# Optimization experiments

Hardware: AMD Instinct MI355X
Metric: run time of the kernel (lower is better)

## Reference

```python
import jax, jax.numpy as jnp
import numpy as np

EPS = 1e-6
T, B, E, H, D, P = 1024, 4, 512, 8, 64, 64  # tgt_len, bsz, embed_dim, heads, head_dim, proj_dim


def setup_inputs() -> dict:
    key = jax.random.key(0)
    ks = jax.random.split(key, 8)
    wscale = (2.0 / (E + E)) ** 0.5  # xavier-ish, gain=init_scale**-0.5=1
    return {
        "x": jax.random.normal(ks[0], (T, B, E), jnp.float32),
        "random_matrices": jax.random.normal(ks[1], (H, P, D), jnp.float32),
        "Wq": jax.random.normal(ks[2], (E, E), jnp.float32) * wscale,
        "bq": jnp.zeros((E,), jnp.float32),
        "Wk": jax.random.normal(ks[3], (E, E), jnp.float32) * wscale,
        "bk": jnp.zeros((E,), jnp.float32),
        "Wv": jax.random.normal(ks[4], (E, E), jnp.float32) * wscale,
        "bv": jnp.zeros((E,), jnp.float32),
        "Wo": jax.random.normal(ks[5], (E, E), jnp.float32) * wscale,
        "bo": jnp.zeros((E,), jnp.float32),
    }


def _phi(x, rm, tau=1.0):
    # RFA trig random features: l2-normalize (scaled by 1/tau), project with
    # per-head random matrices, then [sin, cos] / sqrt(proj_dim).
    # x: [T,B,H,D], rm: [H,P,D] -> [T,B,H,2P]
    xn = x / (tau * jnp.maximum(jnp.linalg.norm(x, axis=-1, keepdims=True), EPS))
    proj = jnp.einsum('tbhd,hpd->tbhp', xn, rm)
    return jnp.concatenate([jnp.sin(proj), jnp.cos(proj)], axis=-1) * (P ** -0.5)


def reference(x, random_matrices, Wq, bq, Wk, bk, Wv, bv, Wo, bo):
    t, b, e = x.shape
    q = (x @ Wq.T + bq).reshape(t, b, H, D)
    k = (x @ Wk.T + bk).reshape(t, b, H, D)
    v = (x @ Wv.T + bv).reshape(t, b, H, D)

    pq = _phi(q, random_matrices)  # [T,B,H,2P]
    pk = _phi(k, random_matrices)  # [T,B,H,2P]

    K = 2 * P
    s0 = jnp.zeros((b, H, K, D), x.dtype)
    z0 = jnp.zeros((b, H, K), x.dtype)

    def step(carry, inp):
        s, z = carry
        pq_t, pk_t, v_t = inp  # [B,H,K], [B,H,K], [B,H,D]
        s = s + pk_t[..., :, None] * v_t[..., None, :]   # outer(phi_k, v)
        z = z + pk_t
        qs = jnp.einsum('bhk,bhkd->bhd', pq_t, s)
        qz = jnp.maximum(jnp.einsum('bhk,bhk->bh', pq_t, z), EPS)
        return (s, z), qs / qz[..., None]

    _, attn = jax.lax.scan(step, (s0, z0), (pq, pk, v))  # attn: [T,B,H,D]
    attn = attn.reshape(t, b, e)
    return attn @ Wo.T + bo
```

## Files before the change

### kernel.cpp

```cpp
#include <hip/hip_runtime.h>

#define T_ 1024
#define B_ 4
#define E_ 512
#define H_ 8
#define D_ 64
#define P_ 64
#define K2 128
#define N_ (T_*B_)
#define CHK 64
#define NC (T_/CHK)
#define BH (B_*H_)
#define EPSV 1e-6f

typedef unsigned int uint;
typedef unsigned short ushort;
typedef short short8 __attribute__((ext_vector_type(8)));
typedef float f32x4 __attribute__((ext_vector_type(4)));

__device__ __forceinline__ float b2f(ushort u){ return __uint_as_float(((uint)u) << 16); }
__device__ __forceinline__ ushort f2b(float f){
  uint x = __float_as_uint(f);
  return (ushort)((x + 0x7fffu + ((x >> 16) & 1u)) >> 16);
}
__device__ __forceinline__ float lo16(uint u){ return __uint_as_float(u << 16); }
__device__ __forceinline__ float hi16(uint u){ return __uint_as_float(u & 0xffff0000u); }
__device__ __forceinline__ void st(float* p, float v){ *p = v; }
__device__ __forceinline__ void st(ushort* p, float v){ *p = f2b(v); }

__device__ __forceinline__ void gl16(const ushort* g, ushort* lds) {
  __builtin_amdgcn_global_load_lds(
      (const __attribute__((address_space(1))) uint*)g,
      (__attribute__((address_space(3))) uint*)lds, 16, 0, 0);
}

__global__ __launch_bounds__(256) void cast_kernel(
    const float* __restrict__ x, const float* __restrict__ wq, const float* __restrict__ wk,
    const float* __restrict__ wv, const float* __restrict__ wo, const float* __restrict__ rm,
    ushort* __restrict__ xb, ushort* __restrict__ wqb, ushort* __restrict__ wkb,
    ushort* __restrict__ wvb, ushort* __restrict__ wob, ushort* __restrict__ rmb)
{
  const float* src; ushort* dst; int n4;
  switch (blockIdx.y) {
    case 0:  src = x;  dst = xb;  n4 = N_ * E_ / 4; break;
    case 1:  src = wq; dst = wqb; n4 = E_ * E_ / 4; break;
    case 2:  src = wk; dst = wkb; n4 = E_ * E_ / 4; break;
    case 3:  src = wv; dst = wvb; n4 = E_ * E_ / 4; break;
    case 4:  src = wo; dst = wob; n4 = E_ * E_ / 4; break;
    default: src = rm; dst = rmb; n4 = H_ * P_ * D_ / 4; break;
  }
  const int stride = gridDim.x * 256;
  for (int i = blockIdx.x * 256 + threadIdx.x; i < n4; i += stride) {
    const float4 v = *(const float4*)(src + (size_t)i * 4);
    ushort4 o; o.x = f2b(v.x); o.y = f2b(v.y); o.z = f2b(v.z); o.w = f2b(v.w);
    *(ushort4*)(dst + (size_t)i * 4) = o;
  }
}

template<typename OutT>
__device__ __forceinline__ void gemm_tile(
    const ushort* __restrict__ A, const ushort* __restrict__ W,
    const float* __restrict__ bias, OutT* __restrict__ out,
    const int row0, const int col0)
{
  __shared__ ushort sA[128 * 32];
  __shared__ ushort sB[64 * 32];
  const int tid = threadIdx.x, w = tid >> 6, lane = tid & 63;
  const int lrow = lane >> 2, lk8 = (lane & 3) * 8;
  const ushort* gA = A + (size_t)(row0 + w * 16 + lrow) * E_ + lk8;
  const ushort* gB = W + (size_t)(col0 + w * 16 + lrow) * E_ + lk8;
  ushort* lA = sA + w * 512;
  ushort* lB = sB + w * 512;
  const int r = lane & 15, kg = lane >> 4, kq = kg * 8;
  f32x4 acc[4][4] = {};
  for (int k0 = 0; k0 < E_; k0 += 32) {
    gl16(gA + k0,             lA);
    gl16(gA + k0 + 32 * E_,   lA + 1024);
    gl16(gA + k0 + 64 * E_,   lA + 2048);
    gl16(gA + k0 + 96 * E_,   lA + 3072);
    gl16(gB + k0,             lB);
    gl16(gB + k0 + 32 * E_,   lB + 1024);
    __syncthreads();
    short8 af[4], bf[4];
    #pragma unroll
    for (int m = 0; m < 4; ++m) af[m] = *(const short8*)(sA + (w * 64 + m * 16 + r) * 32 + kq);
    #pragma unroll
    for (int n = 0; n < 4; ++n) bf[n] = *(const short8*)(sB + (n * 16 + r) * 32 + kq);
    #pragma unroll
    for (int m = 0; m < 4; ++m)
      #pragma unroll
      for (int n = 0; n < 4; ++n)
        acc[m][n] = __builtin_amdgcn_mfma_f32_16x16x32_bf16(af[m], bf[n], acc[m][n], 0, 0, 0);
    __syncthreads();
  }
  float bs[4];
  #pragma unroll
  for (int n = 0; n < 4; ++n) bs[n] = bias[col0 + n * 16 + r];
  #pragma unroll
  for (int m = 0; m < 4; ++m) {
    #pragma unroll
    for (int j = 0; j < 4; ++j) {
      const int row_g = row0 + w * 64 + m * 16 + kg * 4 + j;
      #pragma unroll
      for (int n = 0; n < 4; ++n)
        st(out + (size_t)row_g * E_ + col0 + n * 16 + r, acc[m][n][j] + bs[n]);
    }
  }
}

__global__ __launch_bounds__(128) void gemm_qkv_kernel(
    const ushort* __restrict__ A,
    const ushort* __restrict__ wq, const ushort* __restrict__ wk, const ushort* __restrict__ wv,
    const float* __restrict__ bq, const float* __restrict__ bk, const float* __restrict__ bv,
    ushort* __restrict__ qb, ushort* __restrict__ kb, ushort* __restrict__ vb)
{
  const ushort* W; const float* bias; ushort* dst;
  if (blockIdx.z == 0)      { W = wq; bias = bq; dst = qb; }
  else if (blockIdx.z == 1) { W = wk; bias = bk; dst = kb; }
  else                      { W = wv; bias = bv; dst = vb; }
  gemm_tile<ushort>(A, W, bias, dst, blockIdx.x * 128, blockIdx.y * 64);
}

__global__ __launch_bounds__(128) void gemm_out_kernel(
    const ushort* __restrict__ A, const ushort* __restrict__ W,
    const float* __restrict__ bias, float* __restrict__ out)
{
  gemm_tile<float>(A, W, bias, out, blockIdx.x * 128, blockIdx.y * 64);
}

__global__ __launch_bounds__(256) void phi_kernel(
    const ushort* __restrict__ qb, const ushort* __restrict__ kb,
    const ushort* __restrict__ rmb, ushort* __restrict__ pq, ushort* __restrict__ pk)
{
  __shared__ ushort xq[64][72];
  __shared__ ushort rms[64][72];
  __shared__ float inv_s[64];
  const int tid = threadIdx.x;
  const int h = blockIdx.y;
  const ushort* src = blockIdx.z ? kb : qb;
  ushort* dst = blockIdx.z ? pk : pq;
  const int n0 = blockIdx.x * 64;
  const int row = tid >> 2, seg = (tid & 3) * 16;
  {
    const ushort* gq = src + (size_t)(n0 + row) * E_ + h * D_ + seg;
    const ushort* gr = rmb + ((size_t)h * P_ + row) * D_ + seg;
    const uint4 q0 = *(const uint4*)(gq);
    const uint4 q1 = *(const uint4*)(gq + 8);
    *(uint4*)(&xq[row][seg])      = q0;
    *(uint4*)(&xq[row][seg + 8])  = q1;
    *(uint4*)(&rms[row][seg])     = *(const uint4*)(gr);
    *(uint4*)(&rms[row][seg + 8]) = *(const uint4*)(gr + 8);
    float s2 = 0.f;
    const uint* qw = (const uint*)&q0;
    #pragma unroll
    for (int i = 0; i < 4; ++i) { const float a = lo16(qw[i]), b = hi16(qw[i]); s2 += a*a + b*b; }
    const uint* qw1 = (const uint*)&q1;
    #pragma unroll
    for (int i = 0; i < 4; ++i) { const float a = lo16(qw1[i]), b = hi16(qw1[i]); s2 += a*a + b*b; }
    s2 += __shfl_xor(s2, 1, 64);
    s2 += __shfl_xor(s2, 2, 64);
    if ((tid & 3) == 0) inv_s[row] = 1.0f / fmaxf(sqrtf(s2), EPSV);
  }
  __syncthreads();
  const int w = tid >> 6, lane = tid & 63;
  const int r = lane & 15, kg = lane >> 4;
  const int m0 = w * 16;
  f32x4 acc[4] = {};
  #pragma unroll
  for (int k0 = 0; k0 < D_; k0 += 32) {
    const short8 a = *(const short8*)(&xq[m0 + r][k0 + kg * 8]);
    #pragma unroll
    for (int nt = 0; nt < 4; ++nt) {
      const short8 bfr = *(const short8*)(&rms[nt * 16 + r][k0 + kg * 8]);
      acc[nt] = __builtin_amdgcn_mfma_f32_16x16x32_bf16(a, bfr, acc[nt], 0, 0, 0);
    }
  }
  #pragma unroll
  for (int j = 0; j < 4; ++j) {
    const int rr = m0 + kg * 4 + j;
    const float inv = inv_s[rr];
    const size_t base = ((size_t)(n0 + rr) * H_ + h) * K2;
    #pragma unroll
    for (int nt = 0; nt < 4; ++nt) {
      const int p = nt * 16 + r;
      const float proj = acc[nt][j] * inv;
      dst[base + p]      = f2b(__sinf(proj) * 0.125f);
      dst[base + 64 + p] = f2b(__cosf(proj) * 0.125f);
    }
  }
}

__global__ __launch_bounds__(256) void chunk_sum_kernel(
    const ushort* __restrict__ pk, const ushort* __restrict__ v,
    ushort* __restrict__ cS, float* __restrict__ cz)
{
  const int c = blockIdx.x, bh = blockIdx.y, b = bh >> 3, h = bh & 7;
  __shared__ ushort pkT[K2][88];
  __shared__ ushort vT[D_][88];
  const int tid = threadIdx.x;
  for (int i = tid; i < CHK * 16; i += 256) {
    const int tt = i >> 4, k8 = (i & 15) * 8;
    const int n = (c * CHK + tt) * B_ + b;
    const ushort4 u0 = *(const ushort4*)(pk + ((size_t)n * H_ + h) * K2 + k8);
    const ushort4 u1 = *(const ushort4*)(pk + ((size_t)n * H_ + h) * K2 + k8 + 4);
    pkT[k8+0][tt] = u0.x; pkT[k8+1][tt] = u0.y; pkT[k8+2][tt] = u0.z; pkT[k8+3][tt] = u0.w;
    pkT[k8+4][tt] = u1.x; pkT[k8+5][tt] = u1.y; pkT[k8+6][tt] = u1.z; pkT[k8+7][tt] = u1.w;
  }
  for (int i = tid; i < CHK * 16; i += 256) {
    const int tt = i >> 4, d4 = (i & 15) * 4;
    const int n = (c * CHK + tt) * B_ + b;
    const ushort4 u = *(const ushort4*)(v + (size_t)n * E_ + h * D_ + d4);
    vT[d4+0][tt] = u.x; vT[d4+1][tt] = u.y; vT[d4+2][tt] = u.z; vT[d4+3][tt] = u.w;
  }
  __syncthreads();
  const int w = tid >> 6, lane = tid & 63;
  const int r = lane & 15, kb = lane >> 4;
  const int m0 = w * 32;
  f32x4 acc[2][4] = {};
  #pragma unroll
  for (int k0 = 0; k0 < CHK; k0 += 32) {
    const short8 a0 = *(const short8*)(&pkT[m0 + r][k0 + kb * 8]);
    const short8 a1 = *(const short8*)(&pkT[m0 + 16 + r][k0 + kb * 8]);
    #pragma unroll
    for (int nt = 0; nt < 4; ++nt) {
      const short8 bv = *(const short8*)(&vT[nt * 16 + r][k0 + kb * 8]);
      acc[0][nt] = __builtin_amdgcn_mfma_f32_16x16x32_bf16(a0, bv, acc[0][nt], 0, 0, 0);
      acc[1][nt] = __builtin_amdgcn_mfma_f32_16x16x32_bf16(a1, bv, acc[1][nt], 0, 0, 0);
    }
  }
  ushort* So = cS + (size_t)(c * BH + bh) * (K2 * D_);
  #pragma unroll
  for (int mt = 0; mt < 2; ++mt)
    #pragma unroll
    for (int nt = 0; nt < 4; ++nt)
      #pragma unroll
      for (int j = 0; j < 4; ++j)
        So[(m0 + mt * 16 + kb * 4 + j) * D_ + nt * 16 + r] = f2b(acc[mt][nt][j]);
  if (tid < K2) {
    float zacc = 0.f;
    #pragma unroll
    for (int i2 = 0; i2 < CHK / 2; ++i2) {
      const uint u = *(const uint*)(&pkT[tid][i2 * 2]);
      zacc += lo16(u) + hi16(u);
    }
    cz[(size_t)(c * BH + bh) * K2 + tid] = zacc;
  }
}

__global__ __launch_bounds__(256) void prefix_kernel(
    ushort* __restrict__ cS, float* __restrict__ cz)
{
  const int gid = blockIdx.x * 256 + threadIdx.x;
  const int bh = gid >> 13, rem = gid & 8191;
  float run = 0.f;
  #pragma unroll
  for (int c = 0; c < NC; ++c) {
    ushort* p = cS + (((size_t)(c * BH + bh)) << 13) + rem;
    const float t = b2f(*p); *p = f2b(run); run += t;
  }
  if (gid < BH * K2) {
    const int zbh = gid >> 7, k2 = gid & 127;
    float rz = 0.f;
    #pragma unroll
    for (int c = 0; c < NC; ++c) {
      float* pz = cz + (size_t)(c * BH + zbh) * K2 + k2;
      const float t = *pz; *pz = rz; rz += t;
    }
  }
}

__global__ __launch_bounds__(256) void chunk_out_kernel(
    const ushort* __restrict__ pq, const ushort* __restrict__ pkg,
    const ushort* __restrict__ v, const ushort* __restrict__ Sp,
    const float* __restrict__ zp, ushort* __restrict__ attn)
{
  const int c = blockIdx.x, bh = blockIdx.y, b = bh >> 3, h = bh & 7;
  __shared__ ushort pq_s[CHK][136];
  __shared__ ushort pk_s[CHK][136];
  __shared__ ushort SpT_s[D_][136];
  __shared__ ushort vT_s[D_][88];
  __shared__ ushort Am_s[CHK][88];
  __shared__ float zps[K2];
  __shared__ float dens_s[CHK];
  __shared__ float inv_s[CHK];
  const int tid = threadIdx.x;
  for (int i = tid; i < CHK * 16; i += 256) {
    const int tt = i >> 4, k8 = (i & 15) * 8;
    const int n = (c * CHK + tt) * B_ + b;
    const size_t off = ((size_t)n * H_ + h) * K2 + k8;
    *(uint4*)(&pq_s[tt][k8]) = *(const uint4*)(pq + off);
    *(uint4*)(&pk_s[tt][k8]) = *(const uint4*)(pkg + off);
  }
  for (int i = tid; i < CHK * 16; i += 256) {
    const int tt = i >> 4, d4 = (i & 15) * 4;
    const int n = (c * CHK + tt) * B_ + b;
    const ushort4 u = *(const ushort4*)(v + (size_t)n * E_ + h * D_ + d4);
    vT_s[d4+0][tt] = u.x; vT_s[d4+1][tt] = u.y; vT_s[d4+2][tt] = u.z; vT_s[d4+3][tt] = u.w;
  }
  const ushort* Spb = Sp + (size_t)(c * BH + bh) * (K2 * D_);
  for (int i = tid; i < K2 * 8; i += 256) {
    const int k2 = i >> 3, d8 = (i & 7) * 8;
    const ushort4 s0 = *(const ushort4*)(Spb + k2 * D_ + d8);
    const ushort4 s1 = *(const ushort4*)(Spb + k2 * D_ + d8 + 4);
    SpT_s[d8+0][k2] = s0.x; SpT_s[d8+1][k2] = s0.y;
    SpT_s[d8+2][k2] = s0.z; SpT_s[d8+3][k2] = s0.w;
    SpT_s[d8+4][k2] = s1.x; SpT_s[d8+5][k2] = s1.y;
    SpT_s[d8+6][k2] = s1.z; SpT_s[d8+7][k2] = s1.w;
  }
  if (tid < K2) zps[tid] = zp[(size_t)(c * BH + bh) * K2 + tid];
  __syncthreads();

  const int w = tid >> 6, lane = tid & 63;
  const int r = lane & 15, kb = lane >> 4;
  const int m0 = w * 16;
  f32x4 accA[4] = {};
  #pragma unroll
  for (int k0 = 0; k0 < K2; k0 += 32) {
    const short8 aq = *(const short8*)(&pq_s[m0 + r][k0 + kb * 8]);
    #pragma unroll
    for (int nt = 0; nt < 4; ++nt) {
      const short8 bk = *(const short8*)(&pk_s[nt * 16 + r][k0 + kb * 8]);
      accA[nt] = __builtin_amdgcn_mfma_f32_16x16x32_bf16(aq, bk, accA[nt], 0, 0, 0);
    }
  }
  float rs[4] = {0.f, 0.f, 0.f, 0.f};
  #pragma unroll
  for (int nt = 0; nt < 4; ++nt) {
    #pragma unroll
    for (int j = 0; j < 4; ++j) {
      const int row = kb * 4 + j, col = nt * 16 + r;
      float a = accA[nt][j];
      a = (col <= m0 + row) ? a : 0.f;
      rs[j] += a;
      Am_s[m0 + row][col] = f2b(a);
    }
  }
  #pragma unroll
  for (int off = 1; off < 16; off <<= 1) {
    rs[0] += __shfl_xor(rs[0], off, 64);
    rs[1] += __shfl_xor(rs[1], off, 64);
    rs[2] += __shfl_xor(rs[2], off, 64);
    rs[3] += __shfl_xor(rs[3], off, 64);
  }
  if (r == 0) {
    #pragma unroll
    for (int j = 0; j < 4; ++j) dens_s[m0 + kb * 4 + j] = rs[j];
  }
  f32x4 accO[4] = {};
  #pragma unroll
  for (int k0 = 0; k0 < CHK; k0 += 32) {
    const short8 aa = *(const short8*)(&Am_s[m0 + r][k0 + kb * 8]);
    #pragma unroll
    for (int nt = 0; nt < 4; ++nt) {
      const short8 bv = *(const short8*)(&vT_s[nt * 16 + r][k0 + kb * 8]);
      accO[nt] = __builtin_amdgcn_mfma_f32_16x16x32_bf16(aa, bv, accO[nt], 0, 0, 0);
    }
  }
  #pragma unroll
  for (int k0 = 0; k0 < K2; k0 += 32) {
    const short8 aq = *(const short8*)(&pq_s[m0 + r][k0 + kb * 8]);
    #pragma unroll
    for (int nt = 0; nt < 4; ++nt) {
      const short8 bs = *(const short8*)(&SpT_s[nt * 16 + r][k0 + kb * 8]);
      accO[nt] = __builtin_amdgcn_mfma_f32_16x16x32_bf16(aq, bs, accO[nt], 0, 0, 0);
    }
  }
  {
    const int t_loc = m0 + (lane >> 2), seg = lane & 3;
    float qz = 0.f;
    #pragma unroll
    for (int ii = 0; ii < 16; ++ii) {
      const uint u = *(const uint*)(&pq_s[t_loc][seg * 32 + ii * 2]);
      qz += lo16(u) * zps[seg * 32 + ii * 2] + hi16(u) * zps[seg * 32 + ii * 2 + 1];
    }
    qz += __shfl_xor(qz, 1, 64);
    qz += __shfl_xor(qz, 2, 64);
    if (seg == 0) inv_s[t_loc] = 1.0f / fmaxf(dens_s[t_loc] + qz, EPSV);
  }
  #pragma unroll
  for (int j = 0; j < 4; ++j) {
    const int row = m0 + kb * 4 + j;
    const float inv = inv_s[row];
    const int n = (c * CHK + row) * B_ + b;
    ushort* op = attn + (size_t)n * E_ + h * D_;
    #pragma unroll
    for (int nt = 0; nt < 4; ++nt) op[nt * 16 + r] = f2b(accO[nt][j] * inv);
  }
}

extern "C" void kernel_launch(void* const* d_in, const int* in_sizes, int n_in,
                              void* d_out, int out_size, void* d_ws, size_t ws_size,
                              hipStream_t stream) {
  const float* x  = (const float*)d_in[0];
  const float* rm = (const float*)d_in[1];
  const float* Wq = (const float*)d_in[2];
  const float* bq = (const float*)d_in[3];
  const float* Wk = (const float*)d_in[4];
  const float* bk = (const float*)d_in[5];
  const float* Wv = (const float*)d_in[6];
  const float* bv = (const float*)d_in[7];
  const float* Wo = (const float*)d_in[8];
  const float* bo = (const float*)d_in[9];
  float* out = (float*)d_out;

  ushort* xb  = (ushort*)d_ws;
  ushort* wqb = xb + (size_t)N_ * E_;
  ushort* wkb = wqb + (size_t)E_ * E_;
  ushort* wvb = wkb + (size_t)E_ * E_;
  ushort* wob = wvb + (size_t)E_ * E_;
  ushort* rmb = wob + (size_t)E_ * E_;
  ushort* qb  = rmb + (size_t)H_ * P_ * D_;
  ushort* kb  = qb + (size_t)N_ * E_;
  ushort* vb  = kb + (size_t)N_ * E_;
  ushort* pqb = vb + (size_t)N_ * E_;
  ushort* pkb = pqb + (size_t)N_ * H_ * K2;
  ushort* attnb = pkb + (size_t)N_ * H_ * K2;
  ushort* cS = attnb + (size_t)N_ * E_;
  float* cz = (float*)(cS + (size_t)NC * BH * K2 * D_);

  cast_kernel<<<dim3(512, 6), dim3(256), 0, stream>>>(
      x, Wq, Wk, Wv, Wo, rm, xb, wqb, wkb, wvb, wob, rmb);
  gemm_qkv_kernel<<<dim3(N_ / 128, E_ / 64, 3), dim3(128), 0, stream>>>(
      xb, wqb, wkb, wvb, bq, bk, bv, qb, kb, vb);
  phi_kernel<<<dim3(N_ / 64, H_, 2), dim3(256), 0, stream>>>(qb, kb, rmb, pqb, pkb);
  chunk_sum_kernel<<<dim3(NC, BH), dim3(256), 0, stream>>>(pkb, vb, cS, cz);
  prefix_kernel<<<dim3(1024), dim3(256), 0, stream>>>(cS, cz);
  chunk_out_kernel<<<dim3(NC, BH), dim3(256), 0, stream>>>(pqb, pkb, vb, cS, cz, attnb);
  gemm_out_kernel<<<dim3(N_ / 128, E_ / 64), dim3(128), 0, stream>>>(attnb, wob, bo, out);
}
```

Before: 63.47 us.

## Fuse phi feature map into QKV projection GEMM epilogue

The Q/K projection GEMM now computes the per-head L2 norm and the random-feature projection with sin/cos inside its epilogue. Because each block's 64-column tile is exactly one head, the Q and K intermediates no longer need to be written to global memory and read back. This removes one kernel launch and the global round trip of q and k. In exchange the GEMM kernel uses more shared memory and registers, and the norm is now taken over fp32 values rather than rounded bf16 values.

```diff
diff --git a/kernel.cpp b/kernel.cpp
--- a/kernel.cpp
+++ b/kernel.cpp
@@ -57,14 +57,25 @@
   }
 }
 
-template<typename OutT>
-__device__ __forceinline__ void gemm_tile(
-    const ushort* __restrict__ A, const ushort* __restrict__ W,
-    const float* __restrict__ bias, OutT* __restrict__ out,
-    const int row0, const int col0)
-{
-  __shared__ ushort sA[128 * 32];
-  __shared__ ushort sB[64 * 32];
+__global__ __launch_bounds__(128) void gemm_qkv_phi_kernel(
+    const ushort* __restrict__ A,
+    const ushort* __restrict__ wq, const ushort* __restrict__ wk, const ushort* __restrict__ wv,
+    const float* __restrict__ bq, const float* __restrict__ bk, const float* __restrict__ bv,
+    const ushort* __restrict__ rmb,
+    ushort* __restrict__ vb, ushort* __restrict__ pq, ushort* __restrict__ pk)
+{
+  __shared__ ushort smem[14080];
+  ushort* sA = smem;
+  ushort* sB = smem + 4096;
+  const int z = blockIdx.z;
+  const ushort* W; const float* bias;
+  if (z == 0)      { W = wq; bias = bq; }
+  else if (z == 1) { W = wk; bias = bk; }
+  else             { W = wv; bias = bv; }
+  const int row0 = blockIdx.x * 128;
+  const int h = blockIdx.y;
+  const int col0 = h * 64;
+
   const int tid = threadIdx.x, w = tid >> 6, lane = tid & 63;
   const int lrow = lane >> 2, lk8 = (lane & 3) * 8;
   const ushort* gA = A + (size_t)(row0 + w * 16 + lrow) * E_ + lk8;
@@ -96,98 +107,137 @@
   float bs[4];
   #pragma unroll
   for (int n = 0; n < 4; ++n) bs[n] = bias[col0 + n * 16 + r];
-  #pragma unroll
-  for (int m = 0; m < 4; ++m) {
+
+  if (z == 2) {
+    #pragma unroll
+    for (int m = 0; m < 4; ++m)
+      #pragma unroll
+      for (int j = 0; j < 4; ++j) {
+        const int row_g = row0 + w * 64 + m * 16 + kg * 4 + j;
+        #pragma unroll
+        for (int n = 0; n < 4; ++n)
+          vb[(size_t)row_g * E_ + col0 + n * 16 + r] = f2b(acc[m][n][j] + bs[n]);
+      }
+    return;
+  }
+
+  ushort* qt    = smem;
+  ushort* rms   = smem + 9216;
+  float*  inv_s = (float*)(smem + 13824);
+  {
+    const int rrow = tid >> 1, half = (tid & 1) * 32;
+    const ushort* gr = rmb + ((size_t)h * P_ + rrow) * D_ + half;
+    ushort* dr = rms + rrow * 72 + half;
+    *(uint4*)(dr)      = *(const uint4*)(gr);
+    *(uint4*)(dr + 8)  = *(const uint4*)(gr + 8);
+    *(uint4*)(dr + 16) = *(const uint4*)(gr + 16);
+    *(uint4*)(dr + 24) = *(const uint4*)(gr + 24);
+  }
+  float rs[16];
+  #pragma unroll
+  for (int i = 0; i < 16; ++i) rs[i] = 0.f;
+  #pragma unroll
+  for (int m = 0; m < 4; ++m)
+    #pragma unroll
+    for (int nt = 0; nt < 4; ++nt)
+      #pragma unroll
+      for (int j = 0; j < 4; ++j) {
+        const float val = acc[m][nt][j] + bs[nt];
+        qt[(w * 64 + m * 16 + kg * 4 + j) * 72 + nt * 16 + r] = f2b(val);
+        rs[m * 4 + j] += val * val;
+      }
+  #pragma unroll
+  for (int off = 1; off < 16; off <<= 1)
+    #pragma unroll
+    for (int i = 0; i < 16; ++i) rs[i] += __shfl_xor(rs[i], off, 64);
+  if (r == 0) {
+    #pragma unroll
+    for (int m = 0; m < 4; ++m)
+      #pragma unroll
+      for (int j = 0; j < 4; ++j)
+        inv_s[w * 64 + m * 16 + kg * 4 + j] = 1.0f / fmaxf(sqrtf(rs[m * 4 + j]), EPSV);
+  }
+  __syncthreads();
+  f32x4 acc2[4][4] = {};
+  #pragma unroll
+  for (int k0 = 0; k0 < D_; k0 += 32) {
+    short8 af2[4];
+    #pragma unroll
+    for (int m = 0; m < 4; ++m)
+      af2[m] = *(const short8*)(&qt[(w * 64 + m * 16 + r) * 72 + k0 + kq]);
+    #pragma unroll
+    for (int nt = 0; nt < 4; ++nt) {
+      const short8 bf2 = *(const short8*)(&rms[(nt * 16 + r) * 72 + k0 + kq]);
+      #pragma unroll
+      for (int m = 0; m < 4; ++m)
+        acc2[m][nt] = __builtin_amdgcn_mfma_f32_16x16x32_bf16(af2[m], bf2, acc2[m][nt], 0, 0, 0);
+    }
+  }
+  ushort* dst = z ? pk : pq;
+  #pragma unroll
+  for (int m = 0; m < 4; ++m)
     #pragma unroll
     for (int j = 0; j < 4; ++j) {
-      const int row_g = row0 + w * 64 + m * 16 + kg * 4 + j;
-      #pragma unroll
-      for (int n = 0; n < 4; ++n)
-        st(out + (size_t)row_g * E_ + col0 + n * 16 + r, acc[m][n][j] + bs[n]);
-    }
-  }
-}
-
-__global__ __launch_bounds__(128) void gemm_qkv_kernel(
-    const ushort* __restrict__ A,
-    const ushort* __restrict__ wq, const ushort* __restrict__ wk, const ushort* __restrict__ wv,
-    const float* __restrict__ bq, const float* __restrict__ bk, const float* __restrict__ bv,
-    ushort* __restrict__ qb, ushort* __restrict__ kb, ushort* __restrict__ vb)
-{
-  const ushort* W; const float* bias; ushort* dst;
-  if (blockIdx.z == 0)      { W = wq; bias = bq; dst = qb; }
-  else if (blockIdx.z == 1) { W = wk; bias = bk; dst = kb; }
-  else                      { W = wv; bias = bv; dst = vb; }
-  gemm_tile<ushort>(A, W, bias, dst, blockIdx.x * 128, blockIdx.y * 64);
+      const int row = w * 64 + m * 16 + kg * 4 + j;
+      const float inv = inv_s[row];
+      const size_t base = ((size_t)(row0 + row) * H_ + h) * K2;
+      #pragma unroll
+      for (int nt = 0; nt < 4; ++nt) {
+        const int p = nt * 16 + r;
+        const float proj = acc2[m][nt][j] * inv;
+        dst[base + p]      = f2b(__sinf(proj) * 0.125f);
+        dst[base + 64 + p] = f2b(__cosf(proj) * 0.125f);
+      }
+    }
 }
 
 __global__ __launch_bounds__(128) void gemm_out_kernel(
     const ushort* __restrict__ A, const ushort* __restrict__ W,
     const float* __restrict__ bias, float* __restrict__ out)
 {
-  gemm_tile<float>(A, W, bias, out, blockIdx.x * 128, blockIdx.y * 64);
-}
-
-__global__ __launch_bounds__(256) void phi_kernel(
-    const ushort* __restrict__ qb, const ushort* __restrict__ kb,
-    const ushort* __restrict__ rmb, ushort* __restrict__ pq, ushort* __restrict__ pk)
-{
-  __shared__ ushort xq[64][72];
-  __shared__ ushort rms[64][72];
-  __shared__ float inv_s[64];
-  const int tid = threadIdx.x;
-  const int h = blockIdx.y;
-  const ushort* src = blockIdx.z ? kb : qb;
-  ushort* dst = blockIdx.z ? pk : pq;
-  const int n0 = blockIdx.x * 64;
-  const int row = tid >> 2, seg = (tid & 3) * 16;
-  {
-    const ushort* gq = src + (size_t)(n0 + row) * E_ + h * D_ + seg;
-    const ushort* gr = rmb + ((size_t)h * P_ + row) * D_ + seg;
-    const uint4 q0 = *(const uint4*)(gq);
-    const uint4 q1 = *(const uint4*)(gq + 8);
-    *(uint4*)(&xq[row][seg])      = q0;
-    *(uint4*)(&xq[row][seg + 8])  = q1;
-    *(uint4*)(&rms[row][seg])     = *(const uint4*)(gr);
-    *(uint4*)(&rms[row][seg + 8]) = *(const uint4*)(gr + 8);
-    float s2 = 0.f;
-    const uint* qw = (const uint*)&q0;
-    #pragma unroll
-    for (int i = 0; i < 4; ++i) { const float a = lo16(qw[i]), b = hi16(qw[i]); s2 += a*a + b*b; }
-    const uint* qw1 = (const uint*)&q1;
-    #pragma unroll
-    for (int i = 0; i < 4; ++i) { const float a = lo16(qw1[i]), b = hi16(qw1[i]); s2 += a*a + b*b; }
-    s2 += __shfl_xor(s2, 1, 64);
-    s2 += __shfl_xor(s2, 2, 64);
-    if ((tid & 3) == 0) inv_s[row] = 1.0f / fmaxf(sqrtf(s2), EPSV);
-  }
-  __syncthreads();
-  const int w = tid >> 6, lane = tid & 63;
-  const int r = lane & 15, kg = lane >> 4;
-  const int m0 = w * 16;
-  f32x4 acc[4] = {};
-  #pragma unroll
-  for (int k0 = 0; k0 < D_; k0 += 32) {
-    const short8 a = *(const short8*)(&xq[m0 + r][k0 + kg * 8]);
-    #pragma unroll
-    for (int nt = 0; nt < 4; ++nt) {
-      const short8 bfr = *(const short8*)(&rms[nt * 16 + r][k0 + kg * 8]);
-      acc[nt] = __builtin_amdgcn_mfma_f32_16x16x32_bf16(a, bfr, acc[nt], 0, 0, 0);
-    }
-  }
-  #pragma unroll
-  for (int j = 0; j < 4; ++j) {
-    const int rr = m0 + kg * 4 + j;
-    const float inv = inv_s[rr];
-    const size_t base = ((size_t)(n0 + rr) * H_ + h) * K2;
-    #pragma unroll
-    for (int nt = 0; nt < 4; ++nt) {
-      const int p = nt * 16 + r;
-      const float proj = acc[nt][j] * inv;
-      dst[base + p]      = f2b(__sinf(proj) * 0.125f);
-      dst[base + 64 + p] = f2b(__cosf(proj) * 0.125f);
-    }
-  }
+  __shared__ ushort sA[128 * 32];
+  __shared__ ushort sB[64 * 32];
+  const int tid = threadIdx.x, w = tid >> 6, lane = tid & 63;
+  const int row0 = blockIdx.x * 128, col0 = blockIdx.y * 64;
+  const int lrow = lane >> 2, lk8 = (lane & 3) * 8;
+  const ushort* gA = A + (size_t)(row0 + w * 16 + lrow) * E_ + lk8;
+  const ushort* gB = W + (size_t)(col0 + w * 16 + lrow) * E_ + lk8;
+  ushort* lA = sA + w * 512;
+  ushort* lB = sB + w * 512;
+  const int r = lane & 15, kg = lane >> 4, kq = kg * 8;
+  f32x4 acc[4][4] = {};
+  for (int k0 = 0; k0 < E_; k0 += 32) {
+    gl16(gA + k0,             lA);
+    gl16(gA + k0 + 32 * E_,   lA + 1024);
+    gl16(gA + k0 + 64 * E_,   lA + 2048);
+    gl16(gA + k0 + 96 * E_,   lA + 3072);
+    gl16(gB + k0,             lB);
+    gl16(gB + k0 + 32 * E_,   lB + 1024);
+    __syncthreads();
+    short8 af[4], bf[4];
+    #pragma unroll
+    for (int m = 0; m < 4; ++m) af[m] = *(const short8*)(sA + (w * 64 + m * 16 + r) * 32 + kq);
+    #pragma unroll
+    for (int n = 0; n < 4; ++n) bf[n] = *(const short8*)(sB + (n * 16 + r) * 32 + kq);
+    #pragma unroll
+    for (int m = 0; m < 4; ++m)
+      #pragma unroll
+      for (int n = 0; n < 4; ++n)
+        acc[m][n] = __builtin_amdgcn_mfma_f32_16x16x32_bf16(af[m], bf[n], acc[m][n], 0, 0, 0);
+    __syncthreads();
+  }
+  float bs[4];
+  #pragma unroll
+  for (int n = 0; n < 4; ++n) bs[n] = bias[col0 + n * 16 + r];
+  #pragma unroll
+  for (int m = 0; m < 4; ++m)
+    #pragma unroll
+    for (int j = 0; j < 4; ++j) {
+      const int row_g = row0 + w * 64 + m * 16 + kg * 4 + j;
+      #pragma unroll
+      for (int n = 0; n < 4; ++n)
+        out[(size_t)row_g * E_ + col0 + n * 16 + r] = acc[m][n][j] + bs[n];
+    }
 }
 
 __global__ __launch_bounds__(256) void chunk_sum_kernel(
@@ -409,9 +459,7 @@
   ushort* wvb = wkb + (size_t)E_ * E_;
   ushort* wob = wvb + (size_t)E_ * E_;
   ushort* rmb = wob + (size_t)E_ * E_;
-  ushort* qb  = rmb + (size_t)H_ * P_ * D_;
-  ushort* kb  = qb + (size_t)N_ * E_;
-  ushort* vb  = kb + (size_t)N_ * E_;
+  ushort* vb  = rmb + (size_t)H_ * P_ * D_;
   ushort* pqb = vb + (size_t)N_ * E_;
   ushort* pkb = pqb + (size_t)N_ * H_ * K2;
   ushort* attnb = pkb + (size_t)N_ * H_ * K2;
@@ -420,9 +468,8 @@
 
   cast_kernel<<<dim3(512, 6), dim3(256), 0, stream>>>(
       x, Wq, Wk, Wv, Wo, rm, xb, wqb, wkb, wvb, wob, rmb);
-  gemm_qkv_kernel<<<dim3(N_ / 128, E_ / 64, 3), dim3(128), 0, stream>>>(
-      xb, wqb, wkb, wvb, bq, bk, bv, qb, kb, vb);
-  phi_kernel<<<dim3(N_ / 64, H_, 2), dim3(256), 0, stream>>>(qb, kb, rmb, pqb, pkb);
+  gemm_qkv_phi_kernel<<<dim3(N_ / 128, H_, 3), dim3(128), 0, stream>>>(
+      xb, wqb, wkb, wvb, bq, bk, bv, rmb, vb, pqb, pkb);
   chunk_sum_kernel<<<dim3(NC, BH), dim3(256), 0, stream>>>(pkb, vb, cS, cz);
   prefix_kernel<<<dim3(1024), dim3(256), 0, stream>>>(cS, cz);
   chunk_out_kernel<<<dim3(NC, BH), dim3(256), 0, stream>>>(pqb, pkb, vb, cS, cz, attnb);
```

Measured after the change: 68.47 us. 1.08x slower.

## Fuse chunk-sum, prefix and chunk-output kernels into one cooperative kernel

Applied to the files above, without the earlier changes.

Merges the three chunked linear-attention stages into a single cooperative launch that uses grid-wide barriers between the per-chunk state sums, the cross-chunk prefix scan and the output computation. The aim is to cut two kernel launches and their gaps, and to keep the transposed V tile in shared memory across the stages instead of reloading it. Shared memory is now carved by hand from one buffer, and the prefix work is spread across the 512 blocks. The cost is two grid syncs and the requirement that all 512 blocks be co-resident, which this launch size should satisfy.

```diff
diff --git a/kernel.cpp b/kernel.cpp
--- a/kernel.cpp
+++ b/kernel.cpp
@@ -1,4 +1,7 @@
 #include <hip/hip_runtime.h>
+#include <hip/hip_cooperative_groups.h>
+
+namespace cg = cooperative_groups;
 
 #define T_ 1024
 #define B_ 4
@@ -190,136 +193,136 @@
   }
 }
 
-__global__ __launch_bounds__(256) void chunk_sum_kernel(
-    const ushort* __restrict__ pk, const ushort* __restrict__ v,
-    ushort* __restrict__ cS, float* __restrict__ cz)
-{
+__global__ __launch_bounds__(256) void scan_kernel(
+    const ushort* __restrict__ pq, const ushort* __restrict__ pkg,
+    const ushort* __restrict__ v, ushort* __restrict__ cS,
+    float* __restrict__ cz, ushort* __restrict__ attn)
+{
+  cg::grid_group gridg = cg::this_grid();
+  __shared__ ushort smem[37888];
+  ushort* vT    = smem;
+  ushort* pkT   = smem + 5632;
+  ushort* pq_s  = smem + 5632;
+  ushort* pk_s  = smem + 14336;
+  ushort* SpT_s = smem + 23040;
+  ushort* Am_s  = smem + 31744;
+  float*  zps   = (float*)(smem + 37376);
+  float*  dens_s= zps + 128;
+  float*  inv_s = dens_s + 64;
+
   const int c = blockIdx.x, bh = blockIdx.y, b = bh >> 3, h = bh & 7;
-  __shared__ ushort pkT[K2][88];
-  __shared__ ushort vT[D_][88];
   const int tid = threadIdx.x;
+  const int w = tid >> 6, lane = tid & 63;
+  const int r = lane & 15, kb = lane >> 4;
+
   for (int i = tid; i < CHK * 16; i += 256) {
     const int tt = i >> 4, k8 = (i & 15) * 8;
     const int n = (c * CHK + tt) * B_ + b;
-    const ushort4 u0 = *(const ushort4*)(pk + ((size_t)n * H_ + h) * K2 + k8);
-    const ushort4 u1 = *(const ushort4*)(pk + ((size_t)n * H_ + h) * K2 + k8 + 4);
-    pkT[k8+0][tt] = u0.x; pkT[k8+1][tt] = u0.y; pkT[k8+2][tt] = u0.z; pkT[k8+3][tt] = u0.w;
-    pkT[k8+4][tt] = u1.x; pkT[k8+5][tt] = u1.y; pkT[k8+6][tt] = u1.z; pkT[k8+7][tt] = u1.w;
+    const ushort4 u0 = *(const ushort4*)(pkg + ((size_t)n * H_ + h) * K2 + k8);
+    const ushort4 u1 = *(const ushort4*)(pkg + ((size_t)n * H_ + h) * K2 + k8 + 4);
+    pkT[(k8+0)*88 + tt] = u0.x; pkT[(k8+1)*88 + tt] = u0.y;
+    pkT[(k8+2)*88 + tt] = u0.z; pkT[(k8+3)*88 + tt] = u0.w;
+    pkT[(k8+4)*88 + tt] = u1.x; pkT[(k8+5)*88 + tt] = u1.y;
+    pkT[(k8+6)*88 + tt] = u1.z; pkT[(k8+7)*88 + tt] = u1.w;
   }
   for (int i = tid; i < CHK * 16; i += 256) {
     const int tt = i >> 4, d4 = (i & 15) * 4;
     const int n = (c * CHK + tt) * B_ + b;
     const ushort4 u = *(const ushort4*)(v + (size_t)n * E_ + h * D_ + d4);
-    vT[d4+0][tt] = u.x; vT[d4+1][tt] = u.y; vT[d4+2][tt] = u.z; vT[d4+3][tt] = u.w;
+    vT[(d4+0)*88 + tt] = u.x; vT[(d4+1)*88 + tt] = u.y;
+    vT[(d4+2)*88 + tt] = u.z; vT[(d4+3)*88 + tt] = u.w;
   }
   __syncthreads();
-  const int w = tid >> 6, lane = tid & 63;
-  const int r = lane & 15, kb = lane >> 4;
-  const int m0 = w * 32;
-  f32x4 acc[2][4] = {};
-  #pragma unroll
-  for (int k0 = 0; k0 < CHK; k0 += 32) {
-    const short8 a0 = *(const short8*)(&pkT[m0 + r][k0 + kb * 8]);
-    const short8 a1 = *(const short8*)(&pkT[m0 + 16 + r][k0 + kb * 8]);
-    #pragma unroll
-    for (int nt = 0; nt < 4; ++nt) {
-      const short8 bv = *(const short8*)(&vT[nt * 16 + r][k0 + kb * 8]);
-      acc[0][nt] = __builtin_amdgcn_mfma_f32_16x16x32_bf16(a0, bv, acc[0][nt], 0, 0, 0);
-      acc[1][nt] = __builtin_amdgcn_mfma_f32_16x16x32_bf16(a1, bv, acc[1][nt], 0, 0, 0);
-    }
-  }
-  ushort* So = cS + (size_t)(c * BH + bh) * (K2 * D_);
-  #pragma unroll
-  for (int mt = 0; mt < 2; ++mt)
-    #pragma unroll
-    for (int nt = 0; nt < 4; ++nt)
-      #pragma unroll
-      for (int j = 0; j < 4; ++j)
-        So[(m0 + mt * 16 + kb * 4 + j) * D_ + nt * 16 + r] = f2b(acc[mt][nt][j]);
-  if (tid < K2) {
-    float zacc = 0.f;
-    #pragma unroll
-    for (int i2 = 0; i2 < CHK / 2; ++i2) {
-      const uint u = *(const uint*)(&pkT[tid][i2 * 2]);
-      zacc += lo16(u) + hi16(u);
-    }
-    cz[(size_t)(c * BH + bh) * K2 + tid] = zacc;
-  }
-}
-
-__global__ __launch_bounds__(256) void prefix_kernel(
-    ushort* __restrict__ cS, float* __restrict__ cz)
-{
-  const int gid = blockIdx.x * 256 + threadIdx.x;
-  const int bh = gid >> 13, rem = gid & 8191;
-  float run = 0.f;
-  #pragma unroll
-  for (int c = 0; c < NC; ++c) {
-    ushort* p = cS + (((size_t)(c * BH + bh)) << 13) + rem;
-    const float t = b2f(*p); *p = f2b(run); run += t;
-  }
-  if (gid < BH * K2) {
-    const int zbh = gid >> 7, k2 = gid & 127;
-    float rz = 0.f;
-    #pragma unroll
-    for (int c = 0; c < NC; ++c) {
-      float* pz = cz + (size_t)(c * BH + zbh) * K2 + k2;
-      const float t = *pz; *pz = rz; rz += t;
-    }
-  }
-}
-
-__global__ __launch_bounds__(256) void chunk_out_kernel(
-    const ushort* __restrict__ pq, const ushort* __restrict__ pkg,
-    const ushort* __restrict__ v, const ushort* __restrict__ Sp,
-    const float* __restrict__ zp, ushort* __restrict__ attn)
-{
-  const int c = blockIdx.x, bh = blockIdx.y, b = bh >> 3, h = bh & 7;
-  __shared__ ushort pq_s[CHK][136];
-  __shared__ ushort pk_s[CHK][136];
-  __shared__ ushort SpT_s[D_][136];
-  __shared__ ushort vT_s[D_][88];
-  __shared__ ushort Am_s[CHK][88];
-  __shared__ float zps[K2];
-  __shared__ float dens_s[CHK];
-  __shared__ float inv_s[CHK];
-  const int tid = threadIdx.x;
+  {
+    const int m0s = w * 32;
+    f32x4 acc1[2][4] = {};
+    #pragma unroll
+    for (int k0 = 0; k0 < CHK; k0 += 32) {
+      const short8 a0 = *(const short8*)(&pkT[(m0s + r) * 88 + k0 + kb * 8]);
+      const short8 a1 = *(const short8*)(&pkT[(m0s + 16 + r) * 88 + k0 + kb * 8]);
+      #pragma unroll
+      for (int nt = 0; nt < 4; ++nt) {
+        const short8 bv = *(const short8*)(&vT[(nt * 16 + r) * 88 + k0 + kb * 8]);
+        acc1[0][nt] = __builtin_amdgcn_mfma_f32_16x16x32_bf16(a0, bv, acc1[0][nt], 0, 0, 0);
+        acc1[1][nt] = __builtin_amdgcn_mfma_f32_16x16x32_bf16(a1, bv, acc1[1][nt], 0, 0, 0);
+      }
+    }
+    ushort* So = cS + (size_t)(c * BH + bh) * (K2 * D_);
+    #pragma unroll
+    for (int mt = 0; mt < 2; ++mt)
+      #pragma unroll
+      for (int nt = 0; nt < 4; ++nt)
+        #pragma unroll
+        for (int j = 0; j < 4; ++j)
+          So[(m0s + mt * 16 + kb * 4 + j) * D_ + nt * 16 + r] = f2b(acc1[mt][nt][j]);
+    if (tid < K2) {
+      float zacc = 0.f;
+      #pragma unroll
+      for (int i2 = 0; i2 < CHK / 2; ++i2) {
+        const uint u = *(const uint*)(&pkT[tid * 88 + i2 * 2]);
+        zacc += lo16(u) + hi16(u);
+      }
+      cz[(size_t)(c * BH + bh) * K2 + tid] = zacc;
+    }
+  }
+  gridg.sync();
+
+  {
+    const int fb = blockIdx.y * NC + blockIdx.x;
+    const int gid = fb * 256 + tid;
+    #pragma unroll
+    for (int half = 0; half < 2; ++half) {
+      const int e = gid + half * 131072;
+      const int bh2 = e >> 13, rem = e & 8191;
+      float run = 0.f;
+      #pragma unroll
+      for (int c2 = 0; c2 < NC; ++c2) {
+        ushort* p = cS + (((size_t)(c2 * BH + bh2)) << 13) + rem;
+        const float t = b2f(*p); *p = f2b(run); run += t;
+      }
+    }
+    if (gid < BH * K2) {
+      const int zbh = gid >> 7, k2 = gid & 127;
+      float rz = 0.f;
+      #pragma unroll
+      for (int c2 = 0; c2 < NC; ++c2) {
+        float* pz = cz + (size_t)(c2 * BH + zbh) * K2 + k2;
+        const float t = *pz; *pz = rz; rz += t;
+      }
+    }
+  }
+  gridg.sync();
+
   for (int i = tid; i < CHK * 16; i += 256) {
     const int tt = i >> 4, k8 = (i & 15) * 8;
     const int n = (c * CHK + tt) * B_ + b;
     const size_t off = ((size_t)n * H_ + h) * K2 + k8;
-    *(uint4*)(&pq_s[tt][k8]) = *(const uint4*)(pq + off);
-    *(uint4*)(&pk_s[tt][k8]) = *(const uint4*)(pkg + off);
-  }
-  for (int i = tid; i < CHK * 16; i += 256) {
-    const int tt = i >> 4, d4 = (i & 15) * 4;
-    const int n = (c * CHK + tt) * B_ + b;
-    const ushort4 u = *(const ushort4*)(v + (size_t)n * E_ + h * D_ + d4);
-    vT_s[d4+0][tt] = u.x; vT_s[d4+1][tt] = u.y; vT_s[d4+2][tt] = u.z; vT_s[d4+3][tt] = u.w;
-  }
-  const ushort* Spb = Sp + (size_t)(c * BH + bh) * (K2 * D_);
-  for (int i = tid; i < K2 * 8; i += 256) {
-    const int k2 = i >> 3, d8 = (i & 7) * 8;
-    const ushort4 s0 = *(const ushort4*)(Spb + k2 * D_ + d8);
-    const ushort4 s1 = *(const ushort4*)(Spb + k2 * D_ + d8 + 4);
-    SpT_s[d8+0][k2] = s0.x; SpT_s[d8+1][k2] = s0.y;
-    SpT_s[d8+2][k2] = s0.z; SpT_s[d8+3][k2] = s0.w;
-    SpT_s[d8+4][k2] = s1.x; SpT_s[d8+5][k2] = s1.y;
-    SpT_s[d8+6][k2] = s1.z; SpT_s[d8+7][k2] = s1.w;
-  }
-  if (tid < K2) zps[tid] = zp[(size_t)(c * BH + bh) * K2 + tid];
+    *(uint4*)(&pq_s[tt * 136 + k8]) = *(const uint4*)(pq + off);
+    *(uint4*)(&pk_s[tt * 136 + k8]) = *(const uint4*)(pkg + off);
+  }
+  {
+    const ushort* Spb = cS + (size_t)(c * BH + bh) * (K2 * D_);
+    for (int i = tid; i < K2 * 8; i += 256) {
+      const int k2 = i >> 3, d8 = (i & 7) * 8;
+      const ushort4 s0 = *(const ushort4*)(Spb + k2 * D_ + d8);
+      const ushort4 s1 = *(const ushort4*)(Spb + k2 * D_ + d8 + 4);
+      SpT_s[(d8+0)*136 + k2] = s0.x; SpT_s[(d8+1)*136 + k2] = s0.y;
+      SpT_s[(d8+2)*136 + k2] = s0.z; SpT_s[(d8+3)*136 + k2] = s0.w;
+      SpT_s[(d8+4)*136 + k2] = s1.x; SpT_s[(d8+5)*136 + k2] = s1.y;
+      SpT_s[(d8+6)*136 + k2] = s1.z; SpT_s[(d8+7)*136 + k2] = s1.w;
+    }
+  }
+  if (tid < K2) zps[tid] = cz[(size_t)(c * BH + bh) * K2 + tid];
   __syncthreads();
 
-  const int w = tid >> 6, lane = tid & 63;
-  const int r = lane & 15, kb = lane >> 4;
   const int m0 = w * 16;
   f32x4 accA[4] = {};
   #pragma unroll
   for (int k0 = 0; k0 < K2; k0 += 32) {
-    const short8 aq = *(const short8*)(&pq_s[m0 + r][k0 + kb * 8]);
+    const short8 aq = *(const short8*)(&pq_s[(m0 + r) * 136 + k0 + kb * 8]);
     #pragma unroll
     for (int nt = 0; nt < 4; ++nt) {
-      const short8 bk = *(const short8*)(&pk_s[nt * 16 + r][k0 + kb * 8]);
+      const short8 bk = *(const short8*)(&pk_s[(nt * 16 + r) * 136 + k0 + kb * 8]);
       accA[nt] = __builtin_amdgcn_mfma_f32_16x16x32_bf16(aq, bk, accA[nt], 0, 0, 0);
     }
   }
@@ -332,7 +335,7 @@
       float a = accA[nt][j];
       a = (col <= m0 + row) ? a : 0.f;
       rs[j] += a;
-      Am_s[m0 + row][col] = f2b(a);
+      Am_s[(m0 + row) * 88 + col] = f2b(a);
     }
   }
   #pragma unroll
@@ -349,19 +352,19 @@
   f32x4 accO[4] = {};
   #pragma unroll
   for (int k0 = 0; k0 < CHK; k0 += 32) {
-    const short8 aa = *(const short8*)(&Am_s[m0 + r][k0 + kb * 8]);
+    const short8 aa = *(const short8*)(&Am_s[(m0 + r) * 88 + k0 + kb * 8]);
     #pragma unroll
     for (int nt = 0; nt < 4; ++nt) {
-      const short8 bv = *(const short8*)(&vT_s[nt * 16 + r][k0 + kb * 8]);
+      const short8 bv = *(const short8*)(&vT[(nt * 16 + r) * 88 + k0 + kb * 8]);
       accO[nt] = __builtin_amdgcn_mfma_f32_16x16x32_bf16(aa, bv, accO[nt], 0, 0, 0);
     }
   }
   #pragma unroll
   for (int k0 = 0; k0 < K2; k0 += 32) {
-    const short8 aq = *(const short8*)(&pq_s[m0 + r][k0 + kb * 8]);
+    const short8 aq = *(const short8*)(&pq_s[(m0 + r) * 136 + k0 + kb * 8]);
     #pragma unroll
     for (int nt = 0; nt < 4; ++nt) {
-      const short8 bs = *(const short8*)(&SpT_s[nt * 16 + r][k0 + kb * 8]);
+      const short8 bs = *(const short8*)(&SpT_s[(nt * 16 + r) * 136 + k0 + kb * 8]);
       accO[nt] = __builtin_amdgcn_mfma_f32_16x16x32_bf16(aq, bs, accO[nt], 0, 0, 0);
     }
   }
@@ -370,7 +373,7 @@
     float qz = 0.f;
     #pragma unroll
     for (int ii = 0; ii < 16; ++ii) {
-      const uint u = *(const uint*)(&pq_s[t_loc][seg * 32 + ii * 2]);
+      const uint u = *(const uint*)(&pq_s[t_loc * 136 + seg * 32 + ii * 2]);
       qz += lo16(u) * zps[seg * 32 + ii * 2] + hi16(u) * zps[seg * 32 + ii * 2 + 1];
     }
     qz += __shfl_xor(qz, 1, 64);
@@ -423,8 +426,13 @@
   gemm_qkv_kernel<<<dim3(N_ / 128, E_ / 64, 3), dim3(128), 0, stream>>>(
       xb, wqb, wkb, wvb, bq, bk, bv, qb, kb, vb);
   phi_kernel<<<dim3(N_ / 64, H_, 2), dim3(256), 0, stream>>>(qb, kb, rmb, pqb, pkb);
-  chunk_sum_kernel<<<dim3(NC, BH), dim3(256), 0, stream>>>(pkb, vb, cS, cz);
-  prefix_kernel<<<dim3(1024), dim3(256), 0, stream>>>(cS, cz);
-  chunk_out_kernel<<<dim3(NC, BH), dim3(256), 0, stream>>>(pqb, pkb, vb, cS, cz, attnb);
+  {
+    const ushort* a_pq = pqb; const ushort* a_pk = pkb; const ushort* a_v = vb;
+    ushort* a_cS = cS; float* a_cz = cz; ushort* a_attn = attnb;
+    void* args[6] = { (void*)&a_pq, (void*)&a_pk, (void*)&a_v,
+                      (void*)&a_cS, (void*)&a_cz, (void*)&a_attn };
+    hipLaunchCooperativeKernel((const void*)scan_kernel, dim3(NC, BH), dim3(256),
+                               args, 0, stream);
+  }
   gemm_out_kernel<<<dim3(N_ / 128, E_ / 64), dim3(128), 0, stream>>>(attnb, wob, bo, out);
 }
```

Result: slower. 198.8 us (+213.2%).
